# Performance work log

Measured on AMD Instinct MI355X. Metric: run time of the kernel, lower is better.

The kernel has to match this reference:

```python
import jax, jax.numpy as jnp
import numpy as np


def setup_inputs() -> dict:
    key = jax.random.key(0)
    k1, k2 = jax.random.split(key)
    B, N, M, D = 4, 8192, 8192, 3
    prediction = jax.random.normal(k1, (B, N, D), dtype=jnp.float32)
    target = jax.random.normal(k2, (B, M, D), dtype=jnp.float32)
    return {"prediction": prediction, "target": target}


def reference(prediction, target):
    # prediction: [B, N, 3], target: [B, M, 3] (already channels-last,
    # matching the module's transpose-if-needed behavior).
    x2 = jnp.sum(prediction * prediction, axis=-1)  # [B, N]
    y2 = jnp.sum(target * target, axis=-1)          # [B, M]
    xy = jnp.einsum('bnd,bmd->bnm', prediction, target)  # [B, N, M]
    d2 = x2[:, :, None] + y2[:, None, :] - 2.0 * xy
    d2 = jnp.maximum(d2, 0.0)  # numerical guard
    # pytorch3d chamfer_distance defaults: point_reduction='mean',
    # batch_reduction='mean' -> mean over points per direction, mean over batch,
    # then sum the two directions.
    cham_x = jnp.min(d2, axis=2).mean()  # pred -> target
    cham_y = jnp.min(d2, axis=1).mean()  # target -> pred
    return cham_x + cham_y
```

## Files before the change

kernel.cpp:

```cpp
#include <hip/hip_runtime.h>


#define BLOCK 256
#define RPT   8
#define MC    512
#define NPTS  8192
#define NCH   (NPTS / MC)
#define NB    4

__device__ __forceinline__ float min3f(float a, float b, float c) {
    float d;
    asm("v_min3_f32 %0, %1, %2, %3" : "=v"(d) : "v"(a), "v"(b), "v"(c));
    return d;
}

__global__ __launch_bounds__(BLOCK) void chamfer_min_fused(
    const float* __restrict__ pred, const float* __restrict__ targ,
    float* __restrict__ pA,
    float* __restrict__ pB,
    double* __restrict__ acc, unsigned int* __restrict__ counter) {
    if (blockIdx.x == 0 && blockIdx.y == 0 && blockIdx.z == 0 && threadIdx.x == 0) {
        *acc = 0.0;
        *counter = 0u;
    }

    const int z   = blockIdx.z;
    const int dir = z >> 2, b = z & (NB - 1);
    const float* X = dir ? targ : pred;
    const float* Y = dir ? pred : targ;
    float* partial = dir ? pB : pA;

    __shared__ float4 ldsY[MC];
    const int mc = blockIdx.y;

    for (int p = threadIdx.x; p < MC; p += BLOCK) {
        const float* yp = Y + ((size_t)b * NPTS + (size_t)mc * MC + p) * 3;
        float yx = yp[0], yy = yp[1], yz = yp[2];
        ldsY[p] = make_float4(yx, yy, yz, fmaf(yx, yx, fmaf(yy, yy, yz * yz)));
    }
    __syncthreads();

    const int row0 = blockIdx.x * (BLOCK * RPT);
    float qx[RPT], qy[RPT], qz[RPT], x2[RPT], best[RPT];
#pragma unroll
    for (int r = 0; r < RPT; ++r) {
        int row = row0 + r * BLOCK + threadIdx.x;
        const float* xp = X + ((size_t)b * NPTS + row) * 3;
        float px = xp[0], py = xp[1], pz = xp[2];
        qx[r] = -2.0f * px;
        qy[r] = -2.0f * py;
        qz[r] = -2.0f * pz;
        x2[r] = fmaf(px, px, fmaf(py, py, pz * pz));
        best[r] = 3.0e38f;
    }

    const float4* yptr = ldsY;
#pragma unroll 2
    for (int m = 0; m < MC; m += 4) {
        float4 T0 = yptr[0];
        float4 T1 = yptr[1];
        float4 T2 = yptr[2];
        float4 T3 = yptr[3];
        yptr += 4;
#pragma unroll
        for (int r = 0; r < RPT; ++r) {
            float c0 = fmaf(qx[r], T0.x, fmaf(qy[r], T0.y, fmaf(qz[r], T0.z, T0.w)));
            float c1 = fmaf(qx[r], T1.x, fmaf(qy[r], T1.y, fmaf(qz[r], T1.z, T1.w)));
            float c2 = fmaf(qx[r], T2.x, fmaf(qy[r], T2.y, fmaf(qz[r], T2.z, T2.w)));
            float c3 = fmaf(qx[r], T3.x, fmaf(qy[r], T3.y, fmaf(qz[r], T3.z, T3.w)));
            best[r] = min3f(min3f(best[r], c0, c1), c2, c3);
        }
    }

#pragma unroll
    for (int r = 0; r < RPT; ++r) {
        int row = row0 + r * BLOCK + threadIdx.x;
        partial[((size_t)b * NCH + mc) * NPTS + row] = fmaxf(best[r] + x2[r], 0.0f);
    }
}

__global__ __launch_bounds__(256) void chamfer_reduce(
    const float* __restrict__ pA, const float* __restrict__ pB,
    double* __restrict__ acc, unsigned int* __restrict__ counter,
    float* __restrict__ out) {
    const int g = blockIdx.x * 256 + threadIdx.x;
    const int half = NB * NPTS;
    const float* src = (g < half) ? pA : pB;
    const int gg = g & (half - 1);
    const int b = gg >> 13, r = gg & (NPTS - 1);

    float v = 3.0e38f;
#pragma unroll
    for (int c = 0; c < NCH; ++c)
        v = fminf(v, src[((size_t)b * NCH + c) * NPTS + r]);

    double d = (double)v;
    for (int off = 32; off > 0; off >>= 1) d += __shfl_down(d, off);
    __shared__ double sh[4];
    const int lane = threadIdx.x & 63, wid = threadIdx.x >> 6;
    if (lane == 0) sh[wid] = d;
    __syncthreads();

    if (threadIdx.x == 0) {
        double blocktotal = sh[0] + sh[1] + sh[2] + sh[3];
        atomicAdd(acc, blocktotal);
        __threadfence();
        unsigned int ticket = atomicAdd(counter, 1u);
        if (ticket == gridDim.x - 1) {
            __threadfence();
            double s = atomicAdd(acc, 0.0);
            out[0] = (float)(s / (double)(NB * NPTS));
        }
    }
}

extern "C" void kernel_launch(void* const* d_in, const int* in_sizes, int n_in,
                              void* d_out, int out_size, void* d_ws, size_t ws_size,
                              hipStream_t stream) {
    const float* pred = (const float*)d_in[0];
    const float* targ = (const float*)d_in[1];
    float* out = (float*)d_out;

    float* pA = (float*)d_ws;
    float* pB = pA + (size_t)NB * NCH * NPTS;
    double* acc = (double*)(pB + (size_t)NB * NCH * NPTS);
    unsigned int* counter = (unsigned int*)(acc + 1);

    dim3 g1(NPTS / (BLOCK * RPT), NCH, 2 * NB);
    chamfer_min_fused<<<g1, BLOCK, 0, stream>>>(pred, targ, pA, pB, acc, counter);

    const int nblk = 2 * NB * NPTS / 256;
    chamfer_reduce<<<nblk, 256, 0, stream>>>(pA, pB, acc, counter, out);
}
```

Baseline: 102.8 us.

## Use packed FP32 FMA with paired-point LDS layout and vectorize reduce

```diff
diff --git a/kernel.cpp b/kernel.cpp
--- a/kernel.cpp
+++ b/kernel.cpp
@@ -8,9 +8,18 @@
 #define NCH   (NPTS / MC)
 #define NB    4
 
+typedef float v2f __attribute__((ext_vector_type(2)));
+typedef float v4f __attribute__((ext_vector_type(4)));
+
 __device__ __forceinline__ float min3f(float a, float b, float c) {
     float d;
     asm("v_min3_f32 %0, %1, %2, %3" : "=v"(d) : "v"(a), "v"(b), "v"(c));
+    return d;
+}
+
+__device__ __forceinline__ v2f pk_fma(v2f a, v2f b, v2f c) {
+    v2f d;
+    asm("v_pk_fma_f32 %0, %1, %2, %3" : "=v"(d) : "v"(a), "v"(b), "v"(c));
     return d;
 }
 
@@ -30,45 +39,54 @@
     const float* Y = dir ? pred : targ;
     float* partial = dir ? pB : pA;
 
-    __shared__ float4 ldsY[MC];
+    __shared__ v4f ldsA[MC / 2];
+    __shared__ v4f ldsB[MC / 2];
     const int mc = blockIdx.y;
 
-    for (int p = threadIdx.x; p < MC; p += BLOCK) {
-        const float* yp = Y + ((size_t)b * NPTS + (size_t)mc * MC + p) * 3;
-        float yx = yp[0], yy = yp[1], yz = yp[2];
-        ldsY[p] = make_float4(yx, yy, yz, fmaf(yx, yx, fmaf(yy, yy, yz * yz)));
+    for (int p = threadIdx.x; p < MC / 2; p += BLOCK) {
+        const float* yp = Y + ((size_t)b * NPTS + (size_t)mc * MC + 2 * p) * 3;
+        float ax = yp[0], ay = yp[1], az = yp[2];
+        float bx = yp[3], by = yp[4], bz = yp[5];
+        float aw = fmaf(ax, ax, fmaf(ay, ay, az * az));
+        float bw = fmaf(bx, bx, fmaf(by, by, bz * bz));
+        ldsA[p] = (v4f){ax, bx, ay, by};
+        ldsB[p] = (v4f){az, bz, aw, bw};
     }
     __syncthreads();
 
     const int row0 = blockIdx.x * (BLOCK * RPT);
-    float qx[RPT], qy[RPT], qz[RPT], x2[RPT], best[RPT];
+    v2f qx[RPT], qy[RPT], qz[RPT];
+    float x2[RPT], best[RPT];
 #pragma unroll
     for (int r = 0; r < RPT; ++r) {
         int row = row0 + r * BLOCK + threadIdx.x;
         const float* xp = X + ((size_t)b * NPTS + row) * 3;
         float px = xp[0], py = xp[1], pz = xp[2];
-        qx[r] = -2.0f * px;
-        qy[r] = -2.0f * py;
-        qz[r] = -2.0f * pz;
+        qx[r] = (v2f){-2.0f * px, -2.0f * px};
+        qy[r] = (v2f){-2.0f * py, -2.0f * py};
+        qz[r] = (v2f){-2.0f * pz, -2.0f * pz};
         x2[r] = fmaf(px, px, fmaf(py, py, pz * pz));
         best[r] = 3.0e38f;
     }
 
-    const float4* yptr = ldsY;
 #pragma unroll 2
-    for (int m = 0; m < MC; m += 4) {
-        float4 T0 = yptr[0];
-        float4 T1 = yptr[1];
-        float4 T2 = yptr[2];
-        float4 T3 = yptr[3];
-        yptr += 4;
+    for (int j = 0; j < MC / 2; j += 2) {
+        v4f A0 = ldsA[j],     B0 = ldsB[j];
+        v4f A1 = ldsA[j + 1], B1 = ldsB[j + 1];
+        v2f x01 = __builtin_shufflevector(A0, A0, 0, 1);
+        v2f y01 = __builtin_shufflevector(A0, A0, 2, 3);
+        v2f z01 = __builtin_shufflevector(B0, B0, 0, 1);
+        v2f w01 = __builtin_shufflevector(B0, B0, 2, 3);
+        v2f x23 = __builtin_shufflevector(A1, A1, 0, 1);
+        v2f y23 = __builtin_shufflevector(A1, A1, 2, 3);
+        v2f z23 = __builtin_shufflevector(B1, B1, 0, 1);
+        v2f w23 = __builtin_shufflevector(B1, B1, 2, 3);
 #pragma unroll
         for (int r = 0; r < RPT; ++r) {
-            float c0 = fmaf(qx[r], T0.x, fmaf(qy[r], T0.y, fmaf(qz[r], T0.z, T0.w)));
-            float c1 = fmaf(qx[r], T1.x, fmaf(qy[r], T1.y, fmaf(qz[r], T1.z, T1.w)));
-            float c2 = fmaf(qx[r], T2.x, fmaf(qy[r], T2.y, fmaf(qz[r], T2.z, T2.w)));
-            float c3 = fmaf(qx[r], T3.x, fmaf(qy[r], T3.y, fmaf(qz[r], T3.z, T3.w)));
-            best[r] = min3f(min3f(best[r], c0, c1), c2, c3);
+            v2f c01 = pk_fma(qx[r], x01, pk_fma(qy[r], y01, pk_fma(qz[r], z01, w01)));
+            v2f c23 = pk_fma(qx[r], x23, pk_fma(qy[r], y23, pk_fma(qz[r], z23, w23)));
+            best[r] = min3f(best[r], c01.x, c01.y);
+            best[r] = min3f(best[r], c23.x, c23.y);
         }
     }
 
@@ -84,17 +102,23 @@
     double* __restrict__ acc, unsigned int* __restrict__ counter,
     float* __restrict__ out) {
     const int g = blockIdx.x * 256 + threadIdx.x;
+    const int r4 = g * 4;
     const int half = NB * NPTS;
-    const float* src = (g < half) ? pA : pB;
-    const int gg = g & (half - 1);
+    const float* src = (r4 < half) ? pA : pB;
+    const int gg = r4 & (half - 1);
     const int b = gg >> 13, r = gg & (NPTS - 1);
 
-    float v = 3.0e38f;
+    v4f vb = (v4f){3.0e38f, 3.0e38f, 3.0e38f, 3.0e38f};
 #pragma unroll
-    for (int c = 0; c < NCH; ++c)
-        v = fminf(v, src[((size_t)b * NCH + c) * NPTS + r]);
+    for (int c = 0; c < NCH; ++c) {
+        v4f v = *(const v4f*)(src + ((size_t)b * NCH + c) * NPTS + r);
+        vb.x = fminf(vb.x, v.x);
+        vb.y = fminf(vb.y, v.y);
+        vb.z = fminf(vb.z, v.z);
+        vb.w = fminf(vb.w, v.w);
+    }
 
-    double d = (double)v;
+    double d = (double)vb.x + (double)vb.y + (double)vb.z + (double)vb.w;
     for (int off = 32; off > 0; off >>= 1) d += __shfl_down(d, off);
     __shared__ double sh[4];
     const int lane = threadIdx.x & 63, wid = threadIdx.x >> 6;
@@ -129,6 +153,6 @@
     dim3 g1(NPTS / (BLOCK * RPT), NCH, 2 * NB);
     chamfer_min_fused<<<g1, BLOCK, 0, stream>>>(pred, targ, pA, pB, acc, counter);
 
-    const int nblk = 2 * NB * NPTS / 256;
+    const int nblk = (2 * NB * NPTS / 4) / 256;
     chamfer_reduce<<<nblk, 256, 0, stream>>>(pA, pB, acc, counter, out);
 }
```

Measured after the change: 99.56 us. -3.2%, faster.
